# Optimization experiments

Hardware: AMD Instinct MI355X
Metric: run time of the kernel (lower is better)

## Reference

```python
import jax, jax.numpy as jnp
import numpy as np

NUM_HEADS = 12
KEEP_RATE = 0.7


def setup_inputs() -> dict:
    key = jax.random.key(0)
    ks = jax.random.split(key, 5)
    B, N, C = 64, 197, 768
    x = jax.random.normal(ks[0], (B, N, C), dtype=jnp.float32)
    qkv_w = jax.random.normal(ks[1], (3 * C, C), dtype=jnp.float32) * (C ** -0.5)
    qkv_b = jax.random.normal(ks[2], (3 * C,), dtype=jnp.float32) * 0.02
    proj_w = jax.random.normal(ks[3], (C, C), dtype=jnp.float32) * (C ** -0.5)
    proj_b = jax.random.normal(ks[4], (C,), dtype=jnp.float32) * 0.02
    return {"x": x, "qkv_w": qkv_w, "qkv_b": qkv_b, "proj_w": proj_w, "proj_b": proj_b}


def reference(x, qkv_w, qkv_b, proj_w, proj_b):
    B, N, C = x.shape
    H = NUM_HEADS
    D = C // H
    scale = D ** -0.5
    # qkv projection: [B,N,3C] -> [3,B,H,N,D]
    qkv = (x @ qkv_w.T + qkv_b).reshape(B, N, 3, H, D).transpose(2, 0, 3, 1, 4)
    q, k, v = qkv[0], qkv[1], qkv[2]
    # full materialized attention (required for cls-row extraction)
    attn = jax.nn.softmax(jnp.einsum('bhqd,bhkd->bhqk', q, k) * scale, axis=-1)
    out = jnp.einsum('bhqk,bhkd->bqhd', attn, v).reshape(B, N, C)
    out = out @ proj_w.T + proj_b
    # EViT token pruning: cls-token attention over non-cls keys, head-averaged
    left_tokens = int(KEEP_RATE * (N - 1))  # 137
    cls_attn = attn[:, :, 0, 1:].mean(axis=1)  # [B, N-1]
    _, idx = jax.lax.top_k(cls_attn, left_tokens)  # sorted descending, like torch.topk
    index = jnp.broadcast_to(idx[:, :, None], (B, left_tokens, C))
    return (out, index, idx, cls_attn)
```

## Files before the change

kernel.cpp:

```cpp
#include <hip/hip_runtime.h>
#include <hip/hip_bf16.h>
#include <stdint.h>

constexpr int BATCH = 64;
constexpr int NTOK  = 197;
constexpr int CDIM  = 768;
constexpr int NH    = 12;
constexpr int HD    = 64;
constexpr int MROWS = BATCH * NTOK;
constexpr int MPAD  = 12800;
constexpr int NROWT = MPAD / 128;
constexpr int LEFT  = 137;
constexpr int KPAD  = 224;
constexpr int BH    = BATCH * NH;
constexpr int SPAD  = 208;

constexpr size_t OUT_OFF_OUT   = 0;
constexpr size_t OUT_OFF_INDEX = (size_t)BATCH * NTOK * CDIM;
constexpr size_t OUT_OFF_IDX   = OUT_OFF_INDEX + (size_t)BATCH * LEFT * CDIM;
constexpr size_t OUT_OFF_CLS   = OUT_OFF_IDX + (size_t)BATCH * LEFT;

constexpr size_t WS_CLSPH = 0;
constexpr size_t WS_CLSF  = WS_CLSPH + (size_t)BH * (NTOK - 1);
constexpr size_t WS_IDXI  = WS_CLSF  + (size_t)BATCH * (NTOK - 1);
constexpr size_t WS_Q0    = WS_IDXI  + (size_t)BATCH * LEFT;
constexpr size_t WS_XB    = WS_Q0  + (size_t)BATCH * CDIM;
constexpr size_t WS_WB    = WS_XB  + (size_t)MPAD * CDIM / 2;
constexpr size_t WS_PB    = WS_WB  + (size_t)3 * CDIM * CDIM / 2;
constexpr size_t WS_QB    = WS_PB  + (size_t)CDIM * CDIM / 2;
constexpr size_t WS_KB    = WS_QB  + (size_t)BH * NTOK * HD / 2;
constexpr size_t WS_VTB   = WS_KB  + (size_t)BH * NTOK * HD / 2;
constexpr size_t WS_AOB   = WS_VTB + (size_t)BH * HD * KPAD / 2;
constexpr size_t WS_U     = WS_AOB + (size_t)MPAD * CDIM / 2;
constexpr size_t WS_S     = WS_U   + (size_t)BH * CDIM;

typedef __attribute__((ext_vector_type(8))) short short8;
typedef __attribute__((ext_vector_type(4))) float floatx4;

__device__ __forceinline__ ushort f2bf(float x) {
    __hip_bfloat16 h = __float2bfloat16(x);
    return *(ushort*)&h;
}

__device__ __forceinline__ void load_lds16(const ushort* g, ushort* l) {
    __builtin_amdgcn_global_load_lds(
        (const __attribute__((address_space(1))) uint32_t*)(uintptr_t)g,
        (__attribute__((address_space(3))) uint32_t*)(uint32_t)(uintptr_t)l,
        16, 0, 0);
}

constexpr int X_N4  = MROWS * CDIM / 4;
constexpr int X_NP4 = MPAD * CDIM / 4;
constexpr int W_N4  = 3 * CDIM * CDIM / 4;
constexpr int P_N4  = CDIM * CDIM / 4;
constexpr int CAST_TOTAL = X_NP4 + W_N4 + P_N4;

__global__ __launch_bounds__(256) void cast_all_kernel(const float* __restrict__ x,
                                                       const float* __restrict__ qkv_w,
                                                       const float* __restrict__ proj_w,
                                                       ushort* __restrict__ xb,
                                                       ushort* __restrict__ wb,
                                                       ushort* __restrict__ pb) {
    int i = blockIdx.x * 256 + threadIdx.x;
    const float* src;
    ushort* dst;
    int j, valid;
    if (i < X_NP4) {
        src = x; dst = xb; j = i; valid = (j < X_N4);
    } else if (i < X_NP4 + W_N4) {
        src = qkv_w; dst = wb; j = i - X_NP4; valid = 1;
    } else if (i < CAST_TOTAL) {
        src = proj_w; dst = pb; j = i - X_NP4 - W_N4; valid = 1;
    } else {
        return;
    }
    ushort4 h4 = make_ushort4(0, 0, 0, 0);
    if (valid) {
        float4 a = ((const float4*)src)[j];
        h4 = make_ushort4(f2bf(a.x), f2bf(a.y), f2bf(a.z), f2bf(a.w));
    }
    ((ushort4*)dst)[j] = h4;
}

__global__ __launch_bounds__(256) void q0_kernel(const float* __restrict__ x,
                                                 const float* __restrict__ qkv_w,
                                                 const float* __restrict__ qkv_b,
                                                 float* __restrict__ q0) {
    const int wv   = threadIdx.x >> 6;
    const int lane = threadIdx.x & 63;
    constexpr int CG = CDIM / 4;
    const int b = blockIdx.x / CG;
    const int c = (blockIdx.x - b * CG) * 4 + wv;

    const float* xr = x + (size_t)b * NTOK * CDIM;
    const float* wr = qkv_w + (size_t)c * CDIM;
    float s = 0.f;
#pragma unroll
    for (int i = 0; i < 3; i++) {
        float4 xv = *(const float4*)(xr + lane * 4 + i * 256);
        float4 wv4 = *(const float4*)(wr + lane * 4 + i * 256);
        s += xv.x * wv4.x + xv.y * wv4.y + xv.z * wv4.z + xv.w * wv4.w;
    }
#pragma unroll
    for (int off = 32; off >= 1; off >>= 1) s += __shfl_xor(s, off);
    if (lane == 0) q0[(size_t)b * CDIM + c] = s + qkv_b[c];
}

__global__ __launch_bounds__(256) void u_kernel(const float* __restrict__ q0,
                                                const float* __restrict__ qkv_w,
                                                float* __restrict__ U) {
    const int bh = blockIdx.x;
    const int b  = bh / NH;
    const int h  = bh - b * NH;
    const int t  = threadIdx.x;

    __shared__ float q0s[HD];
    if (t < HD) q0s[t] = q0[(size_t)b * CDIM + h * HD + t];
    __syncthreads();

    const float* wk = qkv_w + (size_t)(CDIM + h * HD) * CDIM;
    float a0 = 0.f, a1 = 0.f, a2 = 0.f;
    for (int d = 0; d < HD; d++) {
        const float qd = q0s[d];
        const float* row = wk + (size_t)d * CDIM;
        a0 = fmaf(qd, row[t],       a0);
        a1 = fmaf(qd, row[t + 256], a1);
        a2 = fmaf(qd, row[t + 512], a2);
    }
    float* ub = U + (size_t)bh * CDIM;
    ub[t] = a0; ub[t + 256] = a1; ub[t + 512] = a2;
}

__global__ __launch_bounds__(256) void score_kernel(const float* __restrict__ x,
                                                    const float* __restrict__ U,
                                                    float* __restrict__ S) {
    const int wv   = threadIdx.x >> 6;
    const int lane = threadIdx.x & 63;
    const int j    = blockIdx.x * 4 + wv;
    const int b    = blockIdx.y;
    if (j >= NTOK) return;

    const float* xr = x + ((size_t)b * NTOK + j) * CDIM;
    float4 xv[3];
#pragma unroll
    for (int i = 0; i < 3; i++) xv[i] = *(const float4*)(xr + lane * 4 + i * 256);

    for (int h = 0; h < NH; h++) {
        const float* ur = U + (size_t)(b * NH + h) * CDIM;
        float s = 0.f;
#pragma unroll
        for (int i = 0; i < 3; i++) {
            float4 uv = *(const float4*)(ur + lane * 4 + i * 256);
            s += xv[i].x * uv.x + xv[i].y * uv.y + xv[i].z * uv.z + xv[i].w * uv.w;
        }
#pragma unroll
        for (int off = 32; off >= 1; off >>= 1) s += __shfl_xor(s, off);
        if (lane == 0) S[(size_t)(b * NH + h) * SPAD + j] = s;
    }
}

template <int MODE, int NCOLT>
__global__ __launch_bounds__(256, 4) void mfma_gemm128(
    const ushort* __restrict__ A, const ushort* __restrict__ W,
    const float* __restrict__ bias,
    float* __restrict__ O0f, ushort* __restrict__ O0q,
    ushort* __restrict__ O1k, ushort* __restrict__ O2vd,
    int Mvalid, int N) {
    constexpr int K   = CDIM;
    constexpr int BK  = 32;
    constexpr int NTK = K / BK;
    __shared__ ushort sA[2 * 128 * BK];
    __shared__ ushort sB[2 * 128 * BK];

    const int t    = threadIdx.x;
    const int lane = t & 63;
    const int w    = t >> 6;
    const int wm   = (w >> 1) * 64;
    const int wn   = (w & 1) * 64;
    const int fr   = lane & 15;
    const int fq   = lane >> 4;
    const int f3   = lane & 3;

    int row, col;
    {
        constexpr int nwg = NROWT * NCOLT;
        constexpr int q = nwg >> 3, r = nwg & 7;
        const int xcd = blockIdx.x & 7, lin = blockIdx.x >> 3;
        const int wg = (xcd < r ? xcd * (q + 1) : r * (q + 1) + (xcd - r) * q) + lin;
        row = wg / NCOLT; col = wg - row * NCOLT;
    }
    const int rowBase = row * 128;
    const int colBase = col * 128;

    auto stage = [&](const ushort* __restrict__ G, ushort* dst, int grow0, int kt) {
#pragma unroll
        for (int i = 0; i < 2; ++i) {
            const int l  = i * 256 + t;
            const int rl = l >> 2;
            const int sl = (l & 3) ^ (rl & 3);
            load_lds16(G + (size_t)(grow0 + rl) * K + kt * BK + sl * 8,
                       dst + l * 8);
        }
    };

    floatx4 acc[4][4];
#pragma unroll
    for (int i = 0; i < 4; ++i)
#pragma unroll
        for (int j = 0; j < 4; ++j)
#pragma unroll
            for (int r2 = 0; r2 < 4; ++r2) acc[i][j][r2] = 0.f;

    const int s0 = (fq ^ f3) * 8;

    stage(A, sA, rowBase, 0);
    stage(W, sB, colBase, 0);

    for (int kt = 0; kt < NTK; ++kt) {
        __syncthreads();
        const int cb = (kt & 1) << 12;
        if (kt + 1 < NTK) {
            stage(A, sA + (cb ^ 4096), rowBase, kt + 1);
            stage(W, sB + (cb ^ 4096), colBase, kt + 1);
        }

        const ushort* pa = sA + cb + (wm + fr) * BK;
        const ushort* pb = sB + cb + (wn + fr) * BK;
        short8 af[4], bf[4];
#pragma unroll
        for (int i = 0; i < 4; ++i) {
            af[i] = *(const short8*)(pa + i * 512 + s0);
            bf[i] = *(const short8*)(pb + i * 512 + s0);
        }
#pragma unroll
        for (int i = 0; i < 4; ++i)
#pragma unroll
            for (int j = 0; j < 4; ++j)
                acc[i][j] = __builtin_amdgcn_mfma_f32_16x16x32_bf16(
                    af[i], bf[j], acc[i][j], 0, 0, 0);
    }

#pragma unroll
    for (int j = 0; j < 4; ++j) {
        const int nn = colBase + wn + j * 16 + fr;
        const float bq = bias[nn];
        if (MODE == 0) {
#pragma unroll
            for (int i = 0; i < 4; ++i) {
                const int mb = rowBase + wm + i * 16 + fq * 4;
#pragma unroll
                for (int r2 = 0; r2 < 4; ++r2) {
                    const int mm = mb + r2;
                    if (mm < Mvalid) O0f[(size_t)mm * N + nn] = acc[i][j][r2] + bq;
                }
            }
        } else {
            const int which = nn / CDIM;
            const int nc    = nn - which * CDIM;
            const int h     = nc >> 6;
            const int d     = nc & 63;
#pragma unroll
            for (int i = 0; i < 4; ++i) {
                const int mb = rowBase + wm + i * 16 + fq * 4;
#pragma unroll
                for (int r2 = 0; r2 < 4; ++r2) {
                    const int mm = mb + r2;
                    if (mm < Mvalid) {
                        const int b   = mm / NTOK;
                        const int tok = mm - b * NTOK;
                        const int bh  = b * NH + h;
                        const ushort val = f2bf(acc[i][j][r2] + bq);
                        if (which == 0)      O0q[((size_t)bh * NTOK + tok) * HD + d] = val;
                        else if (which == 1) O1k[((size_t)bh * NTOK + tok) * HD + d] = val;
                        else                 O2vd[(size_t)mm * CDIM + nc] = val;
                    }
                }
            }
        }
    }
}

__global__ __launch_bounds__(256) void v_transpose_kernel(const ushort* __restrict__ Vd,
                                                          ushort* __restrict__ Vtb) {
    const int bh = blockIdx.x;
    const int b  = bh / NH;
    const int h  = bh - b * NH;
    const int t  = threadIdx.x;

    __shared__ ushort tile[HD][KPAD + 9];

    const int d  = t & 63;
    const int tt = t >> 6;
    const ushort* src = Vd + (size_t)b * NTOK * CDIM + h * HD + d;
    for (int tok0 = 0; tok0 < KPAD; tok0 += 4) {
        const int tok = tok0 + tt;
        ushort v = 0;
        if (tok < NTOK) v = src[(size_t)tok * CDIM];
        tile[d][tok] = v;
    }
    __syncthreads();

    uint* dst = (uint*)(Vtb + (size_t)bh * HD * KPAD);
    constexpr int C2 = KPAD / 2;
    for (int idx = t; idx < HD * C2; idx += 256) {
        const int dd = idx / C2;
        const int c  = idx - dd * C2;
        const uint lo = tile[dd][2 * c];
        const uint hi = tile[dd][2 * c + 1];
        dst[dd * C2 + c] = lo | (hi << 16);
    }
}

constexpr int QTPW = 4;
constexpr int NQG  = 4;

__global__ __launch_bounds__(64) void attn_mfma_kernel(const ushort* __restrict__ Qb,
                                                       const ushort* __restrict__ Kb,
                                                       const ushort* __restrict__ Vtb,
                                                       ushort* __restrict__ AOb) {
    const int g  = blockIdx.x;
    const int bh = blockIdx.y;
    const int b  = bh / NH;
    const int h  = bh - b * NH;
    const int lane = threadIdx.x;
    const int qc   = lane & 15;
    const int quad = lane >> 4;
    const int ntv  = min(QTPW, 13 - g * QTPW);

    __shared__ ushort Pl[QTPW][16][32];
    __shared__ float  alf[QTPW][16], lf[QTPW][16];

    const ushort* Qh = Qb  + (size_t)bh * NTOK * HD;
    const ushort* Kh = Kb  + (size_t)bh * NTOK * HD;
    const ushort* Vh = Vtb + (size_t)bh * HD * KPAD;

    short8 qf[QTPW][2];
#pragma unroll
    for (int ti = 0; ti < QTPW; ++ti) {
        if (ti < ntv) {
            const int qrow = min((g * QTPW + ti) * 16 + qc, NTOK - 1);
            qf[ti][0] = *(const short8*)(Qh + (size_t)qrow * HD + quad * 8);
            qf[ti][1] = *(const short8*)(Qh + (size_t)qrow * HD + 32 + quad * 8);
        }
    }

    floatx4 o[QTPW][4];
#pragma unroll
    for (int ti = 0; ti < QTPW; ++ti)
#pragma unroll
        for (int s = 0; s < 4; ++s)
#pragma unroll
            for (int r = 0; r < 4; ++r) o[ti][s][r] = 0.f;
    float m[QTPW], l[QTPW];
#pragma unroll
    for (int ti = 0; ti < QTPW; ++ti) { m[ti] = -INFINITY; l[ti] = 0.f; }

    for (int c0 = 0; c0 < NTOK; c0 += 32) {
        const int kr0 = min(c0 + qc, NTOK - 1);
        const int kr1 = min(c0 + 16 + qc, NTOK - 1);
        const short8 kf00 = *(const short8*)(Kh + (size_t)kr0 * HD + quad * 8);
        const short8 kf01 = *(const short8*)(Kh + (size_t)kr0 * HD + 32 + quad * 8);
        const short8 kf10 = *(const short8*)(Kh + (size_t)kr1 * HD + quad * 8);
        const short8 kf11 = *(const short8*)(Kh + (size_t)kr1 * HD + 32 + quad * 8);

#pragma unroll
        for (int ti = 0; ti < QTPW; ++ti) {
            if (ti >= ntv) continue;
            floatx4 s0 = {0.f, 0.f, 0.f, 0.f}, s1 = {0.f, 0.f, 0.f, 0.f};
            s0 = __builtin_amdgcn_mfma_f32_16x16x32_bf16(kf00, qf[ti][0], s0, 0, 0, 0);
            s0 = __builtin_amdgcn_mfma_f32_16x16x32_bf16(kf01, qf[ti][1], s0, 0, 0, 0);
            s1 = __builtin_amdgcn_mfma_f32_16x16x32_bf16(kf10, qf[ti][0], s1, 0, 0, 0);
            s1 = __builtin_amdgcn_mfma_f32_16x16x32_bf16(kf11, qf[ti][1], s1, 0, 0, 0);

            float sv[8];
            float mloc = -INFINITY;
#pragma unroll
            for (int r = 0; r < 4; ++r) {
                const int key0 = c0 + quad * 4 + r;
                const int key1 = key0 + 16;
                sv[r]     = (key0 < NTOK) ? s0[r] * 0.125f : -1e30f;
                sv[4 + r] = (key1 < NTOK) ? s1[r] * 0.125f : -1e30f;
                mloc = fmaxf(mloc, fmaxf(sv[r], sv[4 + r]));
            }
            mloc = fmaxf(mloc, __shfl_xor(mloc, 16));
            mloc = fmaxf(mloc, __shfl_xor(mloc, 32));
            const float mnew  = fmaxf(m[ti], mloc);
            const float alpha = __expf(m[ti] - mnew);
            float p[8], ps = 0.f;
#pragma unroll
            for (int i = 0; i < 8; ++i) { p[i] = __expf(sv[i] - mnew); ps += p[i]; }
            ps += __shfl_xor(ps, 16);
            ps += __shfl_xor(ps, 32);
            l[ti] = l[ti] * alpha + ps;
            m[ti] = mnew;

#pragma unroll
            for (int r = 0; r < 4; ++r) {
                Pl[ti][qc][quad * 4 + r]      = f2bf(p[r]);
                Pl[ti][qc][16 + quad * 4 + r] = f2bf(p[4 + r]);
            }
            if (quad == 0) alf[ti][qc] = alpha;
        }
        __syncthreads();

        short8 pf[QTPW];
#pragma unroll
        for (int ti = 0; ti < QTPW; ++ti) {
            if (ti >= ntv) continue;
            pf[ti] = *(const short8*)&Pl[ti][qc][quad * 8];
            float ar[4];
#pragma unroll
            for (int r = 0; r < 4; ++r) ar[r] = alf[ti][quad * 4 + r];
#pragma unroll
            for (int s = 0; s < 4; ++s)
#pragma unroll
                for (int r = 0; r < 4; ++r) o[ti][s][r] *= ar[r];
        }

#pragma unroll
        for (int s = 0; s < 4; ++s) {
            const short8 vf = *(const short8*)(Vh + (size_t)(s * 16 + qc) * KPAD + c0 + quad * 8);
#pragma unroll
            for (int ti = 0; ti < QTPW; ++ti)
                if (ti < ntv)
                    o[ti][s] = __builtin_amdgcn_mfma_f32_16x16x32_bf16(
                        pf[ti], vf, o[ti][s], 0, 0, 0);
        }
        __syncthreads();
    }

#pragma unroll
    for (int ti = 0; ti < QTPW; ++ti)
        if (ti < ntv && quad == 0) lf[ti][qc] = l[ti];
    __syncthreads();

#pragma unroll
    for (int ti = 0; ti < QTPW; ++ti) {
        if (ti >= ntv) continue;
        const int qt = g * QTPW + ti;
#pragma unroll
        for (int r = 0; r < 4; ++r) {
            const int tok = qt * 16 + quad * 4 + r;
            if (tok >= NTOK) continue;
            const float inv = 1.f / lf[ti][quad * 4 + r];
            ushort* dst = AOb + ((size_t)(b * NTOK + tok)) * CDIM + h * HD;
#pragma unroll
            for (int s = 0; s < 4; ++s) dst[s * 16 + qc] = f2bf(o[ti][s][r] * inv);
        }
    }
}

__global__ __launch_bounds__(256) void topk_fused_kernel(const float* __restrict__ S,
                                                         const float* __restrict__ q0,
                                                         const float* __restrict__ qkv_b,
                                                         int* __restrict__ idxI,
                                                         float* __restrict__ idxOut,
                                                         float* __restrict__ outCls) {
    const int b    = blockIdx.x;
    const int t    = threadIdx.x;
    const int lane = t & 63;
    const int w    = t >> 6;

    __shared__ float qbv[NH];
    __shared__ float redm[4], reds[4];
    __shared__ float vsh[NTOK - 1];

    if (w == 0) {
        for (int h = 0; h < NH; ++h) {
            float p = q0[(size_t)b * CDIM + h * HD + lane] * qkv_b[CDIM + h * HD + lane];
#pragma unroll
            for (int off = 32; off >= 1; off >>= 1) p += __shfl_xor(p, off);
            if (lane == 0) qbv[h] = p;
        }
    }
    __syncthreads();

    float macc = 0.f;
    for (int h = 0; h < NH; ++h) {
        const float qb = qbv[h];
        const float sv = (t < NTOK) ? (S[(size_t)(b * NH + h) * SPAD + t] + qb) * 0.125f
                                    : -INFINITY;
        float mloc = sv;
#pragma unroll
        for (int off = 32; off >= 1; off >>= 1) mloc = fmaxf(mloc, __shfl_xor(mloc, off));
        if (lane == 0) redm[w] = mloc;
        __syncthreads();
        const float mx = fmaxf(fmaxf(redm[0], redm[1]), fmaxf(redm[2], redm[3]));
        const float p = (t < NTOK) ? expf(sv - mx) : 0.f;
        float ls = p;
#pragma unroll
        for (int off = 32; off >= 1; off >>= 1) ls += __shfl_xor(ls, off);
        if (lane == 0) reds[w] = ls;
        __syncthreads();
        const float denom = (reds[0] + reds[1]) + (reds[2] + reds[3]);
        macc += p / denom;
        __syncthreads();
    }

    if (t >= 1 && t < NTOK) {
        const float val = macc * (1.f / 12.f);
        vsh[t - 1] = val;
        outCls[(size_t)b * (NTOK - 1) + (t - 1)] = val;
    }
    __syncthreads();

    if (t < NTOK - 1) {
        const float vi = vsh[t];
        int rank = 0;
        for (int j = 0; j < NTOK - 1; j++) {
            const float vj = vsh[j];
            rank += (vj > vi) || (vj == vi && j < t);
        }
        if (rank < LEFT) {
            idxI[b * LEFT + rank]   = t;
            idxOut[b * LEFT + rank] = (float)t;
        }
    }
}

__global__ void fill_index_kernel(const int* __restrict__ idxI,
                                  float* __restrict__ dst) {
    int tid = blockIdx.x * 256 + threadIdx.x;
    constexpr int C4 = CDIM / 4;
    if (tid >= BATCH * LEFT * C4) return;
    float v = (float)idxI[tid / C4];
    ((float4*)dst)[tid] = make_float4(v, v, v, v);
}

extern "C" void kernel_launch(void* const* d_in, const int* in_sizes, int n_in,
                              void* d_out, int out_size, void* d_ws, size_t ws_size,
                              hipStream_t stream) {
    const float* x      = (const float*)d_in[0];
    const float* qkv_w  = (const float*)d_in[1];
    const float* qkv_b  = (const float*)d_in[2];
    const float* proj_w = (const float*)d_in[3];
    const float* proj_b = (const float*)d_in[4];
    float* out = (float*)d_out;

    float*  ws    = (float*)d_ws;
    int*    idxi  = (int*)(ws + WS_IDXI);
    float*  q0    = ws + WS_Q0;
    ushort* xb    = (ushort*)(ws + WS_XB);
    ushort* wb    = (ushort*)(ws + WS_WB);
    ushort* pb    = (ushort*)(ws + WS_PB);
    ushort* qb    = (ushort*)(ws + WS_QB);
    ushort* kb    = (ushort*)(ws + WS_KB);
    ushort* vtb   = (ushort*)(ws + WS_VTB);
    ushort* aob   = (ushort*)(ws + WS_AOB);
    ushort* vd    = aob;
    float*  U     = ws + WS_U;
    float*  S     = ws + WS_S;

    cast_all_kernel<<<CAST_TOTAL / 256, 256, 0, stream>>>(x, qkv_w, proj_w, xb, wb, pb);

    q0_kernel<<<BATCH * (CDIM / 4), 256, 0, stream>>>(x, qkv_w, qkv_b, q0);
    u_kernel<<<BH, 256, 0, stream>>>(q0, qkv_w, U);
    score_kernel<<<dim3((NTOK + 3) / 4, BATCH), 256, 0, stream>>>(x, U, S);

    mfma_gemm128<1, 18><<<NROWT * 18, 256, 0, stream>>>(
        xb, wb, qkv_b, nullptr, qb, kb, vd, MROWS, 3 * CDIM);

    v_transpose_kernel<<<BH, 256, 0, stream>>>(vd, vtb);

    attn_mfma_kernel<<<dim3(NQG, BH), 64, 0, stream>>>(qb, kb, vtb, aob);

    mfma_gemm128<0, 6><<<NROWT * 6, 256, 0, stream>>>(
        aob, pb, proj_b, out + OUT_OFF_OUT, nullptr, nullptr, nullptr,
        MROWS, CDIM);

    topk_fused_kernel<<<BATCH, 256, 0, stream>>>(S, q0, qkv_b, idxi,
                                                 out + OUT_OFF_IDX,
                                                 out + OUT_OFF_CLS);

    fill_index_kernel<<<((size_t)BATCH * LEFT * (CDIM / 4) + 255) / 256, 256, 0, stream>>>(
        idxi, out + OUT_OFF_INDEX);
}
```

Measured before the change: 360.2 us.

## Fold V transpose into attention kernel and q0 into U kernel

The v_transpose kernel is removed. The attention kernel now runs one 256-thread block per (batch, head): it loads V transposed into LDS once, and four waves split the 13 query tiles. Separately, the q0 projection and the q·bias dot product move into u_kernel, which drops the q0 kernel and the per-head reduction in topk. Two launches and the global round trip of transposed V go away, at the cost of only 768 attention blocks and redundant recomputation of q0 inside u_kernel. The workspace is also reassigned: V now goes to the old transposed-V buffer instead of aliasing the attention output.

```diff
diff --git a/kernel.cpp b/kernel.cpp
--- a/kernel.cpp
+++ b/kernel.cpp
@@ -82,41 +82,47 @@
     ((ushort4*)dst)[j] = h4;
 }
 
-__global__ __launch_bounds__(256) void q0_kernel(const float* __restrict__ x,
-                                                 const float* __restrict__ qkv_w,
-                                                 const float* __restrict__ qkv_b,
-                                                 float* __restrict__ q0) {
-    const int wv   = threadIdx.x >> 6;
-    const int lane = threadIdx.x & 63;
-    constexpr int CG = CDIM / 4;
-    const int b = blockIdx.x / CG;
-    const int c = (blockIdx.x - b * CG) * 4 + wv;
-
-    const float* xr = x + (size_t)b * NTOK * CDIM;
-    const float* wr = qkv_w + (size_t)c * CDIM;
-    float s = 0.f;
-#pragma unroll
-    for (int i = 0; i < 3; i++) {
-        float4 xv = *(const float4*)(xr + lane * 4 + i * 256);
-        float4 wv4 = *(const float4*)(wr + lane * 4 + i * 256);
-        s += xv.x * wv4.x + xv.y * wv4.y + xv.z * wv4.z + xv.w * wv4.w;
-    }
-#pragma unroll
-    for (int off = 32; off >= 1; off >>= 1) s += __shfl_xor(s, off);
-    if (lane == 0) q0[(size_t)b * CDIM + c] = s + qkv_b[c];
-}
-
-__global__ __launch_bounds__(256) void u_kernel(const float* __restrict__ q0,
+__global__ __launch_bounds__(256) void u_kernel(const float* __restrict__ x,
                                                 const float* __restrict__ qkv_w,
-                                                float* __restrict__ U) {
+                                                const float* __restrict__ qkv_b,
+                                                float* __restrict__ U,
+                                                float* __restrict__ qbW) {
     const int bh = blockIdx.x;
     const int b  = bh / NH;
     const int h  = bh - b * NH;
     const int t  = threadIdx.x;
-
+    const int wv   = t >> 6;
+    const int lane = t & 63;
+
+    __shared__ float x0s[CDIM];
     __shared__ float q0s[HD];
-    if (t < HD) q0s[t] = q0[(size_t)b * CDIM + h * HD + t];
+
+    if (t < 192) ((float4*)x0s)[t] = ((const float4*)(x + (size_t)b * NTOK * CDIM))[t];
     __syncthreads();
+
+    for (int i = 0; i < 16; ++i) {
+        const int cl = wv * 16 + i;
+        const int c  = h * HD + cl;
+        const float* wr = qkv_w + (size_t)c * CDIM;
+        float s = 0.f;
+#pragma unroll
+        for (int k = 0; k < 3; ++k) {
+            float4 xv  = *(const float4*)(x0s + lane * 4 + k * 256);
+            float4 wv4 = *(const float4*)(wr  + lane * 4 + k * 256);
+            s += xv.x * wv4.x + xv.y * wv4.y + xv.z * wv4.z + xv.w * wv4.w;
+        }
+#pragma unroll
+        for (int off = 32; off >= 1; off >>= 1) s += __shfl_xor(s, off);
+        if (lane == 0) q0s[cl] = s + qkv_b[c];
+    }
+    __syncthreads();
+
+    if (wv == 0) {
+        float p = q0s[lane] * qkv_b[CDIM + h * HD + lane];
+#pragma unroll
+        for (int off = 32; off >= 1; off >>= 1) p += __shfl_xor(p, off);
+        if (lane == 0) qbW[bh] = p;
+    }
 
     const float* wk = qkv_w + (size_t)(CDIM + h * HD) * CDIM;
     float a0 = 0.f, a1 = 0.f, a2 = 0.f;
@@ -280,80 +286,64 @@
     }
 }
 
-__global__ __launch_bounds__(256) void v_transpose_kernel(const ushort* __restrict__ Vd,
-                                                          ushort* __restrict__ Vtb) {
+__global__ __launch_bounds__(256) void attn_mfma_kernel(const ushort* __restrict__ Qb,
+                                                        const ushort* __restrict__ Kb,
+                                                        const ushort* __restrict__ Vd,
+                                                        ushort* __restrict__ AOb) {
     const int bh = blockIdx.x;
     const int b  = bh / NH;
     const int h  = bh - b * NH;
     const int t  = threadIdx.x;
-
-    __shared__ ushort tile[HD][KPAD + 9];
-
-    const int d  = t & 63;
-    const int tt = t >> 6;
-    const ushort* src = Vd + (size_t)b * NTOK * CDIM + h * HD + d;
-    for (int tok0 = 0; tok0 < KPAD; tok0 += 4) {
-        const int tok = tok0 + tt;
-        ushort v = 0;
-        if (tok < NTOK) v = src[(size_t)tok * CDIM];
-        tile[d][tok] = v;
-    }
-    __syncthreads();
-
-    uint* dst = (uint*)(Vtb + (size_t)bh * HD * KPAD);
-    constexpr int C2 = KPAD / 2;
-    for (int idx = t; idx < HD * C2; idx += 256) {
-        const int dd = idx / C2;
-        const int c  = idx - dd * C2;
-        const uint lo = tile[dd][2 * c];
-        const uint hi = tile[dd][2 * c + 1];
-        dst[dd * C2 + c] = lo | (hi << 16);
-    }
-}
-
-constexpr int QTPW = 4;
-constexpr int NQG  = 4;
-
-__global__ __launch_bounds__(64) void attn_mfma_kernel(const ushort* __restrict__ Qb,
-                                                       const ushort* __restrict__ Kb,
-                                                       const ushort* __restrict__ Vtb,
-                                                       ushort* __restrict__ AOb) {
-    const int g  = blockIdx.x;
-    const int bh = blockIdx.y;
-    const int b  = bh / NH;
-    const int h  = bh - b * NH;
-    const int lane = threadIdx.x;
+    const int wv   = t >> 6;
+    const int lane = t & 63;
     const int qc   = lane & 15;
     const int quad = lane >> 4;
-    const int ntv  = min(QTPW, 13 - g * QTPW);
-
-    __shared__ ushort Pl[QTPW][16][32];
-    __shared__ float  alf[QTPW][16], lf[QTPW][16];
-
-    const ushort* Qh = Qb  + (size_t)bh * NTOK * HD;
-    const ushort* Kh = Kb  + (size_t)bh * NTOK * HD;
-    const ushort* Vh = Vtb + (size_t)bh * HD * KPAD;
-
-    short8 qf[QTPW][2];
-#pragma unroll
-    for (int ti = 0; ti < QTPW; ++ti) {
+
+    constexpr int VSTR = KPAD + 8;
+    __shared__ ushort Vt[HD][VSTR];
+    __shared__ ushort Pl[4][4][16][32];
+    __shared__ float  alf[4][4][16], lf[4][4][16];
+
+    {
+        const int d  = t & 63;
+        const int tt = t >> 6;
+        const ushort* src = Vd + (size_t)b * NTOK * CDIM + h * HD + d;
+        for (int tok0 = 0; tok0 < KPAD; tok0 += 4) {
+            const int tok = tok0 + tt;
+            ushort v = 0;
+            if (tok < NTOK) v = src[(size_t)tok * CDIM];
+            Vt[d][tok] = v;
+        }
+    }
+
+    const ushort* Qh = Qb + (size_t)bh * NTOK * HD;
+    const ushort* Kh = Kb + (size_t)bh * NTOK * HD;
+
+    const int tile0 = (wv == 0) ? 0 : 4 + (wv - 1) * 3;
+    const int ntv   = (wv == 0) ? 4 : 3;
+
+    short8 qf[4][2];
+#pragma unroll
+    for (int ti = 0; ti < 4; ++ti) {
         if (ti < ntv) {
-            const int qrow = min((g * QTPW + ti) * 16 + qc, NTOK - 1);
+            const int qrow = min((tile0 + ti) * 16 + qc, NTOK - 1);
             qf[ti][0] = *(const short8*)(Qh + (size_t)qrow * HD + quad * 8);
             qf[ti][1] = *(const short8*)(Qh + (size_t)qrow * HD + 32 + quad * 8);
         }
     }
 
-    floatx4 o[QTPW][4];
-#pragma unroll
-    for (int ti = 0; ti < QTPW; ++ti)
+    floatx4 o[4][4];
+#pragma unroll
+    for (int ti = 0; ti < 4; ++ti)
 #pragma unroll
         for (int s = 0; s < 4; ++s)
 #pragma unroll
             for (int r = 0; r < 4; ++r) o[ti][s][r] = 0.f;
-    float m[QTPW], l[QTPW];
-#pragma unroll
-    for (int ti = 0; ti < QTPW; ++ti) { m[ti] = -INFINITY; l[ti] = 0.f; }
+    float m[4], l[4];
+#pragma unroll
+    for (int ti = 0; ti < 4; ++ti) { m[ti] = -INFINITY; l[ti] = 0.f; }
+
+    __syncthreads();
 
     for (int c0 = 0; c0 < NTOK; c0 += 32) {
         const int kr0 = min(c0 + qc, NTOK - 1);
@@ -364,7 +354,7 @@
         const short8 kf11 = *(const short8*)(Kh + (size_t)kr1 * HD + 32 + quad * 8);
 
 #pragma unroll
-        for (int ti = 0; ti < QTPW; ++ti) {
+        for (int ti = 0; ti < 4; ++ti) {
             if (ti >= ntv) continue;
             floatx4 s0 = {0.f, 0.f, 0.f, 0.f}, s1 = {0.f, 0.f, 0.f, 0.f};
             s0 = __builtin_amdgcn_mfma_f32_16x16x32_bf16(kf00, qf[ti][0], s0, 0, 0, 0);
@@ -396,21 +386,21 @@
 
 #pragma unroll
             for (int r = 0; r < 4; ++r) {
-                Pl[ti][qc][quad * 4 + r]      = f2bf(p[r]);
-                Pl[ti][qc][16 + quad * 4 + r] = f2bf(p[4 + r]);
+                Pl[wv][ti][qc][quad * 4 + r]      = f2bf(p[r]);
+                Pl[wv][ti][qc][16 + quad * 4 + r] = f2bf(p[4 + r]);
             }
-            if (quad == 0) alf[ti][qc] = alpha;
+            if (quad == 0) alf[wv][ti][qc] = alpha;
         }
         __syncthreads();
 
-        short8 pf[QTPW];
-#pragma unroll
-        for (int ti = 0; ti < QTPW; ++ti) {
+        short8 pf[4];
+#pragma unroll
+        for (int ti = 0; ti < 4; ++ti) {
             if (ti >= ntv) continue;
-            pf[ti] = *(const short8*)&Pl[ti][qc][quad * 8];
+            pf[ti] = *(const short8*)&Pl[wv][ti][qc][quad * 8];
             float ar[4];
 #pragma unroll
-            for (int r = 0; r < 4; ++r) ar[r] = alf[ti][quad * 4 + r];
+            for (int r = 0; r < 4; ++r) ar[r] = alf[wv][ti][quad * 4 + r];
 #pragma unroll
             for (int s = 0; s < 4; ++s)
 #pragma unroll
@@ -419,9 +409,9 @@
 
 #pragma unroll
         for (int s = 0; s < 4; ++s) {
-            const short8 vf = *(const short8*)(Vh + (size_t)(s * 16 + qc) * KPAD + c0 + quad * 8);
-#pragma unroll
-            for (int ti = 0; ti < QTPW; ++ti)
+            const short8 vf = *(const short8*)&Vt[s * 16 + qc][c0 + quad * 8];
+#pragma unroll
+            for (int ti = 0; ti < 4; ++ti)
                 if (ti < ntv)
                     o[ti][s] = __builtin_amdgcn_mfma_f32_16x16x32_bf16(
                         pf[ti], vf, o[ti][s], 0, 0, 0);
@@ -430,19 +420,19 @@
     }
 
 #pragma unroll
-    for (int ti = 0; ti < QTPW; ++ti)
-        if (ti < ntv && quad == 0) lf[ti][qc] = l[ti];
+    for (int ti = 0; ti < 4; ++ti)
+        if (ti < ntv && quad == 0) lf[wv][ti][qc] = l[ti];
     __syncthreads();
 
 #pragma unroll
-    for (int ti = 0; ti < QTPW; ++ti) {
+    for (int ti = 0; ti < 4; ++ti) {
         if (ti >= ntv) continue;
-        const int qt = g * QTPW + ti;
+        const int qt = tile0 + ti;
 #pragma unroll
         for (int r = 0; r < 4; ++r) {
             const int tok = qt * 16 + quad * 4 + r;
             if (tok >= NTOK) continue;
-            const float inv = 1.f / lf[ti][quad * 4 + r];
+            const float inv = 1.f / lf[wv][ti][quad * 4 + r];
             ushort* dst = AOb + ((size_t)(b * NTOK + tok)) * CDIM + h * HD;
 #pragma unroll
             for (int s = 0; s < 4; ++s) dst[s * 16 + qc] = f2bf(o[ti][s][r] * inv);
@@ -451,8 +441,7 @@
 }
 
 __global__ __launch_bounds__(256) void topk_fused_kernel(const float* __restrict__ S,
-                                                         const float* __restrict__ q0,
-                                                         const float* __restrict__ qkv_b,
+                                                         const float* __restrict__ qbW,
                                                          int* __restrict__ idxI,
                                                          float* __restrict__ idxOut,
                                                          float* __restrict__ outCls) {
@@ -465,14 +454,7 @@
     __shared__ float redm[4], reds[4];
     __shared__ float vsh[NTOK - 1];
 
-    if (w == 0) {
-        for (int h = 0; h < NH; ++h) {
-            float p = q0[(size_t)b * CDIM + h * HD + lane] * qkv_b[CDIM + h * HD + lane];
-#pragma unroll
-            for (int off = 32; off >= 1; off >>= 1) p += __shfl_xor(p, off);
-            if (lane == 0) qbv[h] = p;
-        }
-    }
+    if (t < NH) qbv[t] = qbW[b * NH + t];
     __syncthreads();
 
     float macc = 0.f;
@@ -539,36 +521,32 @@
 
     float*  ws    = (float*)d_ws;
     int*    idxi  = (int*)(ws + WS_IDXI);
-    float*  q0    = ws + WS_Q0;
+    float*  qbW   = ws + WS_Q0;
     ushort* xb    = (ushort*)(ws + WS_XB);
     ushort* wb    = (ushort*)(ws + WS_WB);
     ushort* pb    = (ushort*)(ws + WS_PB);
     ushort* qb    = (ushort*)(ws + WS_QB);
     ushort* kb    = (ushort*)(ws + WS_KB);
-    ushort* vtb   = (ushort*)(ws + WS_VTB);
+    ushort* vd    = (ushort*)(ws + WS_VTB);
     ushort* aob   = (ushort*)(ws + WS_AOB);
-    ushort* vd    = aob;
     float*  U     = ws + WS_U;
     float*  S     = ws + WS_S;
 
     cast_all_kernel<<<CAST_TOTAL / 256, 256, 0, stream>>>(x, qkv_w, proj_w, xb, wb, pb);
 
-    q0_kernel<<<BATCH * (CDIM / 4), 256, 0, stream>>>(x, qkv_w, qkv_b, q0);
-    u_kernel<<<BH, 256, 0, stream>>>(q0, qkv_w, U);
+    u_kernel<<<BH, 256, 0, stream>>>(x, qkv_w, qkv_b, U, qbW);
     score_kernel<<<dim3((NTOK + 3) / 4, BATCH), 256, 0, stream>>>(x, U, S);
 
     mfma_gemm128<1, 18><<<NROWT * 18, 256, 0, stream>>>(
         xb, wb, qkv_b, nullptr, qb, kb, vd, MROWS, 3 * CDIM);
 
-    v_transpose_kernel<<<BH, 256, 0, stream>>>(vd, vtb);
-
-    attn_mfma_kernel<<<dim3(NQG, BH), 64, 0, stream>>>(qb, kb, vtb, aob);
+    attn_mfma_kernel<<<BH, 256, 0, stream>>>(qb, kb, vd, aob);
 
     mfma_gemm128<0, 6><<<NROWT * 6, 256, 0, stream>>>(
         aob, pb, proj_b, out + OUT_OFF_OUT, nullptr, nullptr, nullptr,
         MROWS, CDIM);
 
-    topk_fused_kernel<<<BATCH, 256, 0, stream>>>(S, q0, qkv_b, idxi,
+    topk_fused_kernel<<<BATCH, 256, 0, stream>>>(S, qbW, idxi,
                                                  out + OUT_OFF_IDX,
                                                  out + OUT_OFF_CLS);
 
```

After: 326.9 us. 9.3% less time.
